# Kernel optimization log

Measured on AMD Instinct MI355X. Metric: run time of the kernel, lower is better.

The kernel has to match this reference:

```python
import jax, jax.numpy as jnp
import numpy as np

B, S, D, H = 2, 2048, 1024, 16
DH = D // H
SCALE = 1.0 / float(np.sqrt(DH))


def setup_inputs() -> dict:
    key = jax.random.key(0)
    ks = jax.random.split(key, 9)
    std = 1.0 / float(np.sqrt(D))
    x = jax.random.normal(ks[0], (B, S, D), dtype=jnp.float32)
    # causal mask: True = masked (future positions)
    mask = jnp.triu(jnp.ones((S, S), dtype=bool), k=1)
    Wq = jax.random.normal(ks[1], (D, D), dtype=jnp.float32) * std
    Wk = jax.random.normal(ks[2], (D, D), dtype=jnp.float32) * std
    Wv = jax.random.normal(ks[3], (D, D), dtype=jnp.float32) * std
    Wo = jax.random.normal(ks[4], (D, D), dtype=jnp.float32) * std
    bq = jax.random.normal(ks[5], (D,), dtype=jnp.float32) * 0.01
    bk = jax.random.normal(ks[6], (D,), dtype=jnp.float32) * 0.01
    bv = jax.random.normal(ks[7], (D,), dtype=jnp.float32) * 0.01
    bo = jax.random.normal(ks[8], (D,), dtype=jnp.float32) * 0.01
    return {"x": x, "mask": mask, "Wq": Wq, "bq": bq, "Wk": Wk, "bk": bk,
            "Wv": Wv, "bv": bv, "Wo": Wo, "bo": bo}


def _split_heads(t):
    # (B, S, D) -> (B, H, S, DH)
    return t.reshape(B, S, H, DH).transpose(0, 2, 1, 3)


def reference(x, mask, Wq, bq, Wk, bk, Wv, bv, Wo, bo):
    # torch nn.Linear: y = x @ W.T + b
    q = _split_heads(x @ Wq.T + bq)
    k = _split_heads(x @ Wk.T + bk)
    v = _split_heads(x @ Wv.T + bv)
    # scores: (B, H, S, S)
    scores = jnp.einsum('bhsd,bhtd->bhst', q, k) * SCALE
    scores = jnp.where(mask[None, None, :, :], jnp.float32(-1e9), scores)
    attn = jax.nn.softmax(scores, axis=-1)
    attn = jnp.nan_to_num(attn, nan=0.0)
    out = jnp.einsum('bhst,bhtd->bhsd', attn, v)
    out = out.transpose(0, 2, 1, 3).reshape(B, S, D)
    return out @ Wo.T + bo
```

## Files before the change

kernel.cpp:

```cpp
#include <hip/hip_runtime.h>

#define S_LEN  2048
#define DMODEL 1024
#define NHEAD  16
#define DHEAD  64
#define SCALE_F 0.125f

typedef unsigned short ushort_t;
typedef __attribute__((ext_vector_type(8))) short bf16x8;
typedef __attribute__((ext_vector_type(4))) float f32x4;

typedef __attribute__((address_space(1))) void gv_t;
typedef __attribute__((address_space(3))) void lv_t;

__device__ __forceinline__ ushort_t f2bf(float f) {
    unsigned u = __builtin_bit_cast(unsigned, f);
    unsigned r = (u + 0x7FFFu + ((u >> 16) & 1u)) >> 16;
    return (ushort_t)r;
}

__device__ __forceinline__ void gload16(const ushort_t* g, ushort_t* l) {
    __builtin_amdgcn_global_load_lds((gv_t*)g, (lv_t*)l, 16, 0, 0);
}

__global__ void cast_all(const float* __restrict__ x,
                         const float* __restrict__ Wq, const float* __restrict__ Wk,
                         const float* __restrict__ Wv, const float* __restrict__ Wo,
                         ushort_t* __restrict__ dst, int n4) {
    int i = blockIdx.x * blockDim.x + threadIdx.x;
    int stride = gridDim.x * blockDim.x;
    for (int idx = i; idx < n4; idx += stride) {
        const float* src; int off;
        if (idx < 1048576)      { src = x;  off = idx; }
        else if (idx < 1310720) { src = Wq; off = idx - 1048576; }
        else if (idx < 1572864) { src = Wk; off = idx - 1310720; }
        else if (idx < 1835008) { src = Wv; off = idx - 1572864; }
        else                    { src = Wo; off = idx - 1835008; }
        float4 f = ((const float4*)src)[off];
        ushort4 o;
        o.x = f2bf(f.x); o.y = f2bf(f.y); o.z = f2bf(f.z); o.w = f2bf(f.w);
        ((ushort4*)dst)[idx] = o;
    }
}

template<int MODE, int BM>
__launch_bounds__(256)
__global__ void gemm_bt(const ushort_t* __restrict__ A, const ushort_t* __restrict__ Bw,
                        const float* __restrict__ b0, const float* __restrict__ b1,
                        const float* __restrict__ b2,
                        void* __restrict__ out0, void* __restrict__ out1, void* __restrict__ out2,
                        int M, int N, int K) {
    constexpr int MF = BM / 32;
    __shared__ ushort_t As[2][BM][32];
    __shared__ ushort_t Bs[2][128][32];
    const int tid  = threadIdx.x;
    const int lane = tid & 63;
    const int w    = tid >> 6;
    const int wr   = w >> 1, wc = w & 1;
    const int m0   = blockIdx.x * BM;
    const int n0   = blockIdx.y * 128;
    const int l15  = lane & 15;
    const int lg   = lane >> 4;
    const int srow = lane >> 2;
    const int scol = (lane & 3) * 8;

    f32x4 acc[MF][4] = {};

    auto stage = [&](int buf, int k0) {
#pragma unroll
        for (int j = 0; j < BM / 64; j++) {
            const int rbase = w * (BM / 4) + j * 16;
            gload16(A + (size_t)(m0 + rbase + srow) * K + k0 + scol, &As[buf][rbase][0]);
        }
#pragma unroll
        for (int j = 0; j < 2; j++) {
            const int rbase = w * 32 + j * 16;
            gload16(Bw + (size_t)(n0 + rbase + srow) * K + k0 + scol, &Bs[buf][rbase][0]);
        }
    };

    stage(0, 0);
    __syncthreads();
    int buf = 0;

    for (int k0 = 0; k0 < K; k0 += 32) {
        if (k0 + 32 < K) stage(buf ^ 1, k0 + 32);
        bf16x8 af[MF], bfr[4];
#pragma unroll
        for (int i = 0; i < MF; i++) af[i]  = *(const bf16x8*)&As[buf][wr*(BM/2) + i*16 + l15][lg*8];
#pragma unroll
        for (int i = 0; i < 4;  i++) bfr[i] = *(const bf16x8*)&Bs[buf][wc*64 + i*16 + l15][lg*8];
#pragma unroll
        for (int mf = 0; mf < MF; mf++)
#pragma unroll
            for (int nf = 0; nf < 4; nf++)
                acc[mf][nf] = __builtin_amdgcn_mfma_f32_16x16x32_bf16(af[mf], bfr[nf], acc[mf][nf], 0, 0, 0);
        __syncthreads();
        buf ^= 1;
    }

#pragma unroll
    for (int mf = 0; mf < MF; mf++) {
#pragma unroll
        for (int nf = 0; nf < 4; nf++) {
            const int col = n0 + wc*64 + nf*16 + l15;
            if constexpr (MODE == 2) {
                const float bv = b0[col];
#pragma unroll
                for (int r = 0; r < 4; r++) {
                    const int row = m0 + wr*(BM/2) + mf*16 + lg*4 + r;
                    ((float*)out0)[(size_t)row * N + col] = acc[mf][nf][r] + bv;
                }
            } else {
                const int mat = col >> 10;
                const int c   = col & 1023;
                const int h   = c >> 6, dh = c & 63;
                const float* bp = (mat == 0) ? b0 : ((mat == 1) ? b1 : b2);
                const float bv = bp[c];
#pragma unroll
                for (int r = 0; r < 4; r++) {
                    const int row = m0 + wr*(BM/2) + mf*16 + lg*4 + r;
                    const int b = row >> 11, s = row & 2047;
                    const float v = acc[mf][nf][r] + bv;
                    if (mat == 0)
                        ((ushort_t*)out0)[((size_t)(b*NHEAD + h) * S_LEN + s) * DHEAD + dh] = f2bf(v);
                    else if (mat == 1)
                        ((ushort_t*)out1)[((size_t)(b*NHEAD + h) * S_LEN + s) * DHEAD + dh] = f2bf(v);
                    else
                        ((ushort_t*)out2)[((size_t)(b*NHEAD + h) * DHEAD + dh) * S_LEN + s] = f2bf(v);
                }
            }
        }
    }
}

__launch_bounds__(256, 3)
__global__ void attn_fwd(const ushort_t* __restrict__ Q, const ushort_t* __restrict__ Kh,
                         const ushort_t* __restrict__ Vt, ushort_t* __restrict__ Aout) {
    __shared__ ushort_t Ks[2][64][64];
    __shared__ ushort_t Vs[2][64][64];
    __shared__ ushort_t Ps[4][16][72];
    const int tid  = threadIdx.x;
    const int lane = tid & 63;
    const int w    = tid >> 6;
    const int l15  = lane & 15, lg = lane >> 4;
    const int bh   = blockIdx.y;
    const int qta  = blockIdx.x;
    const int qtb  = 31 - qta;
    const size_t qkbase = (size_t)bh * S_LEN * DHEAD;
    const size_t vtbase = (size_t)bh * DHEAD * S_LEN;
    const float SL2E = SCALE_F * 1.44269504f;

    const int rsub = lane >> 3;
    const int csw  = ((lane & 7) ^ rsub) * 8;
    const int swz  = (l15 & 7) * 8;

    const int qa = qta * 64 + w * 16;
    const int qb = qtb * 64 + w * 16;

    bf16x8 aqA[2], aqB[2];
#pragma unroll
    for (int kc = 0; kc < 2; kc++) {
        aqA[kc] = *(const bf16x8*)(Q + qkbase + (size_t)(qa + l15) * DHEAD + kc*32 + lg*8);
        aqB[kc] = *(const bf16x8*)(Q + qkbase + (size_t)(qb + l15) * DHEAD + kc*32 + lg*8);
    }

    float mA = -3.0e38f, lA = 0.0f, mB = -3.0e38f, lB = 0.0f;
    f32x4 oA[4] = {}, oB[4] = {};

    auto stage = [&](int buf, int t) {
        const int kv0 = t * 64;
        const ushort_t* kp = Kh + qkbase + (size_t)kv0 * DHEAD;
        const ushort_t* vp = Vt + vtbase + kv0;
#pragma unroll
        for (int j2 = 0; j2 < 2; j2++) {
            const int j  = w * 2 + j2;
            const int rg = j * 8 + rsub;
            gload16(kp + (size_t)rg * DHEAD + csw, &Ks[buf][j*8][0]);
            gload16(vp + (size_t)rg * S_LEN + csw, &Vs[buf][j*8][0]);
        }
    };

    auto compute = [&](int buf, int t, int qbase, bf16x8 (&aq)[2], float& m, float& l,
                       f32x4 (&o)[4], bool domask) {
        const int kv0  = t * 64;
        const int rowq = qbase + l15;
        f32x4 sacc[4] = {};
        __builtin_amdgcn_s_setprio(1);
#pragma unroll
        for (int kc = 0; kc < 2; kc++)
#pragma unroll
            for (int nf = 0; nf < 4; nf++) {
                bf16x8 bk = *(const bf16x8*)&Ks[buf][nf*16 + l15][(kc*32 + lg*8) ^ swz];
                sacc[nf] = __builtin_amdgcn_mfma_f32_16x16x32_bf16(bk, aq[kc], sacc[nf], 0, 0, 0);
            }
        __builtin_amdgcn_s_setprio(0);

        float mx = -3.0e38f;
        if (domask) {
#pragma unroll
            for (int nf = 0; nf < 4; nf++)
#pragma unroll
                for (int r = 0; r < 4; r++) {
                    const int colk = kv0 + nf*16 + lg*4 + r;
                    float v = sacc[nf][r] * SL2E;
                    v = (colk > rowq) ? -3.0e38f : v;
                    sacc[nf][r] = v;
                    mx = fmaxf(mx, v);
                }
        } else {
#pragma unroll
            for (int nf = 0; nf < 4; nf++)
#pragma unroll
                for (int r = 0; r < 4; r++) {
                    const float v = sacc[nf][r] * SL2E;
                    sacc[nf][r] = v;
                    mx = fmaxf(mx, v);
                }
        }
        mx = fmaxf(mx, __shfl_xor(mx, 16));
        mx = fmaxf(mx, __shfl_xor(mx, 32));

        const bool skip = __all(mx <= m + 8.0f);
        const float mn = skip ? m : fmaxf(m, mx);

        float s = 0.0f;
#pragma unroll
        for (int nf = 0; nf < 4; nf++) {
            ushort_t pk[4];
#pragma unroll
            for (int r = 0; r < 4; r++) {
                const float p = exp2f(sacc[nf][r] - mn);
                s += p;
                pk[r] = f2bf(p);
            }
            *(ushort4*)&Ps[w][l15][nf*16 + lg*4] = *(ushort4*)pk;
        }
        s += __shfl_xor(s, 16);
        s += __shfl_xor(s, 32);

        if (skip) {
            l += s;
        } else {
            const float corr = exp2f(m - mn);
            m = mn;
            l = l * corr + s;
            float cf[4];
#pragma unroll
            for (int r = 0; r < 4; r++) cf[r] = __shfl(corr, lg*4 + r);
#pragma unroll
            for (int nf = 0; nf < 4; nf++)
#pragma unroll
                for (int r = 0; r < 4; r++) o[nf][r] *= cf[r];
        }

        __builtin_amdgcn_s_setprio(1);
#pragma unroll
        for (int kc = 0; kc < 2; kc++) {
            bf16x8 pa = *(const bf16x8*)&Ps[w][l15][kc*32 + lg*8];
#pragma unroll
            for (int nf = 0; nf < 4; nf++) {
                bf16x8 bv = *(const bf16x8*)&Vs[buf][nf*16 + l15][(kc*32 + lg*8) ^ swz];
                o[nf] = __builtin_amdgcn_mfma_f32_16x16x32_bf16(pa, bv, o[nf], 0, 0, 0);
            }
        }
        __builtin_amdgcn_s_setprio(0);
    };

    stage(0, 0);
    __syncthreads();
    int buf = 0;

    for (int t = 0; t <= qta; t++) {
        if (t < qtb) stage(buf ^ 1, t + 1);
        compute(buf, t, qa, aqA, mA, lA, oA, t == qta);
        compute(buf, t, qb, aqB, mB, lB, oB, false);
        __syncthreads();
        buf ^= 1;
    }
    for (int t = qta + 1; t <= qtb; t++) {
        if (t < qtb) stage(buf ^ 1, t + 1);
        compute(buf, t, qb, aqB, mB, lB, oB, t == qtb);
        __syncthreads();
        buf ^= 1;
    }

    const int b = bh >> 4, h = bh & 15;
    const float invA = 1.0f / lA, invB = 1.0f / lB;
#pragma unroll
    for (int r = 0; r < 4; r++) {
        const float ia = __shfl(invA, lg*4 + r);
        const float ib = __shfl(invB, lg*4 + r);
        const int rowa = qa + lg*4 + r;
        const int rowb = qb + lg*4 + r;
#pragma unroll
        for (int nf = 0; nf < 4; nf++) {
            Aout[((size_t)(b * S_LEN) + rowa) * DMODEL + h*DHEAD + nf*16 + l15] = f2bf(oA[nf][r] * ia);
            Aout[((size_t)(b * S_LEN) + rowb) * DMODEL + h*DHEAD + nf*16 + l15] = f2bf(oB[nf][r] * ib);
        }
    }
}

extern "C" void kernel_launch(void* const* d_in, const int* in_sizes, int n_in,
                              void* d_out, int out_size, void* d_ws, size_t ws_size,
                              hipStream_t stream) {
    (void)in_sizes; (void)n_in; (void)out_size; (void)ws_size;
    const float* x  = (const float*)d_in[0];
    const float* Wq = (const float*)d_in[2];
    const float* bq = (const float*)d_in[3];
    const float* Wk = (const float*)d_in[4];
    const float* bk = (const float*)d_in[5];
    const float* Wv = (const float*)d_in[6];
    const float* bv = (const float*)d_in[7];
    const float* Wo = (const float*)d_in[8];
    const float* bo = (const float*)d_in[9];

    char* ws = (char*)d_ws;
    ushort_t* xb    = (ushort_t*)(ws);
    ushort_t* Wqkvb = (ushort_t*)(ws + (8u  << 20));
    ushort_t* Wob   = (ushort_t*)(ws + (14u << 20));
    ushort_t* Qh    = (ushort_t*)(ws + (16u << 20));
    ushort_t* Kh    = (ushort_t*)(ws + (24u << 20));
    ushort_t* Vth   = (ushort_t*)(ws + (32u << 20));
    ushort_t* Ao    = (ushort_t*)(ws + (40u << 20));

    cast_all<<<2048, 256, 0, stream>>>(x, Wq, Wk, Wv, Wo, xb, 2097152);

    gemm_bt<0, 128><<<dim3(32, 24), 256, 0, stream>>>(xb, Wqkvb, bq, bk, bv,
                                                      Qh, Kh, Vth, 2*S_LEN, 3*DMODEL, DMODEL);

    attn_fwd<<<dim3(16, 2*NHEAD), 256, 0, stream>>>(Qh, Kh, Vth, Ao);

    gemm_bt<2, 64><<<dim3(64, 8), 256, 0, stream>>>(Ao, Wob, bo, nullptr, nullptr,
                                                    d_out, nullptr, nullptr, 2*S_LEN, DMODEL, DMODEL);
}
```

Before: 127.7 us.

## Split paired causal query tiles into separate blocks with interleaved scheduling

The attention kernel previously gave each block two query tiles (a and 31-a) to balance causal work. It now launches one block per query tile on a 32x32 grid, ordering tiles so heavy and light ones alternate, and raises the occupancy hint to 4. The softmax scale times log2(e) is folded into Q inside the QKV GEMM epilogue. The P tile drops its padding in favour of an XOR swizzle, and P is packed with v_cvt_pk_bf16_f32. Each block now reloads K/V for its own tile instead of sharing them across two tiles, and the order in which blocks are dispatched now decides load balance.

```diff
diff --git a/kernel.cpp b/kernel.cpp
--- a/kernel.cpp
+++ b/kernel.cpp
@@ -5,6 +5,7 @@
 #define NHEAD  16
 #define DHEAD  64
 #define SCALE_F 0.125f
+#define SL2E_F 0.180336880f
 
 typedef unsigned short ushort_t;
 typedef __attribute__((ext_vector_type(8))) short bf16x8;
@@ -17,6 +18,12 @@
     unsigned u = __builtin_bit_cast(unsigned, f);
     unsigned r = (u + 0x7FFFu + ((u >> 16) & 1u)) >> 16;
     return (ushort_t)r;
+}
+
+__device__ __forceinline__ unsigned cvtpk_bf16(float a, float b) {
+    unsigned r;
+    asm("v_cvt_pk_bf16_f32 %0, %1, %2" : "=v"(r) : "v"(a), "v"(b));
+    return r;
 }
 
 __device__ __forceinline__ void gload16(const ushort_t* g, ushort_t* l) {
@@ -121,10 +128,11 @@
                 for (int r = 0; r < 4; r++) {
                     const int row = m0 + wr*(BM/2) + mf*16 + lg*4 + r;
                     const int b = row >> 11, s = row & 2047;
-                    const float v = acc[mf][nf][r] + bv;
-                    if (mat == 0)
+                    float v = acc[mf][nf][r] + bv;
+                    if (mat == 0) {
+                        v *= SL2E_F;
                         ((ushort_t*)out0)[((size_t)(b*NHEAD + h) * S_LEN + s) * DHEAD + dh] = f2bf(v);
-                    else if (mat == 1)
+                    } else if (mat == 1)
                         ((ushort_t*)out1)[((size_t)(b*NHEAD + h) * S_LEN + s) * DHEAD + dh] = f2bf(v);
                     else
                         ((ushort_t*)out2)[((size_t)(b*NHEAD + h) * DHEAD + dh) * S_LEN + s] = f2bf(v);
@@ -134,39 +142,39 @@
     }
 }
 
-__launch_bounds__(256, 3)
+__launch_bounds__(256, 4)
 __global__ void attn_fwd(const ushort_t* __restrict__ Q, const ushort_t* __restrict__ Kh,
                          const ushort_t* __restrict__ Vt, ushort_t* __restrict__ Aout) {
     __shared__ ushort_t Ks[2][64][64];
     __shared__ ushort_t Vs[2][64][64];
-    __shared__ ushort_t Ps[4][16][72];
+    __shared__ ushort_t Ps[4][16][64];
     const int tid  = threadIdx.x;
     const int lane = tid & 63;
     const int w    = tid >> 6;
     const int l15  = lane & 15, lg = lane >> 4;
-    const int bh   = blockIdx.y;
-    const int qta  = blockIdx.x;
-    const int qtb  = 31 - qta;
+    const int bh   = blockIdx.x;
+    const int y    = blockIdx.y;
+    const int kq   = y >> 3, g0 = y & 7;
+    const int qt   = (kq == 0) ? 2*g0 : (kq == 1) ? (31 - 2*g0)
+                   : (kq == 2) ? (2*g0 + 1) : (30 - 2*g0);
+
     const size_t qkbase = (size_t)bh * S_LEN * DHEAD;
     const size_t vtbase = (size_t)bh * DHEAD * S_LEN;
-    const float SL2E = SCALE_F * 1.44269504f;
-
-    const int rsub = lane >> 3;
-    const int csw  = ((lane & 7) ^ rsub) * 8;
-    const int swz  = (l15 & 7) * 8;
-
-    const int qa = qta * 64 + w * 16;
-    const int qb = qtb * 64 + w * 16;
-
-    bf16x8 aqA[2], aqB[2];
-#pragma unroll
-    for (int kc = 0; kc < 2; kc++) {
-        aqA[kc] = *(const bf16x8*)(Q + qkbase + (size_t)(qa + l15) * DHEAD + kc*32 + lg*8);
-        aqB[kc] = *(const bf16x8*)(Q + qkbase + (size_t)(qb + l15) * DHEAD + kc*32 + lg*8);
-    }
-
-    float mA = -3.0e38f, lA = 0.0f, mB = -3.0e38f, lB = 0.0f;
-    f32x4 oA[4] = {}, oB[4] = {};
+
+    const int rsub  = lane >> 3;
+    const int csw   = ((lane & 7) ^ rsub) * 8;
+    const int swz   = (l15 & 7) * 8;
+    const int psxor = (l15 & 7) << 4;
+
+    const int qw = qt * 64 + w * 16;
+
+    bf16x8 aq[2];
+#pragma unroll
+    for (int kc = 0; kc < 2; kc++)
+        aq[kc] = *(const bf16x8*)(Q + qkbase + (size_t)(qw + l15) * DHEAD + kc*32 + lg*8);
+
+    float m = -3.0e38f, l = 0.0f;
+    f32x4 o[4] = {};
 
     auto stage = [&](int buf, int t) {
         const int kv0 = t * 64;
@@ -181,10 +189,16 @@
         }
     };
 
-    auto compute = [&](int buf, int t, int qbase, bf16x8 (&aq)[2], float& m, float& l,
-                       f32x4 (&o)[4], bool domask) {
-        const int kv0  = t * 64;
-        const int rowq = qbase + l15;
+    ushort_t* psw = &Ps[w][0][0];
+    char* psrow = (char*)(psw + l15 * 64);
+
+    stage(0, 0);
+    __syncthreads();
+    int buf = 0;
+
+    for (int t = 0; t <= qt; t++) {
+        if (t < qt) stage(buf ^ 1, t + 1);
+
         f32x4 sacc[4] = {};
         __builtin_amdgcn_s_setprio(1);
 #pragma unroll
@@ -196,46 +210,43 @@
             }
         __builtin_amdgcn_s_setprio(0);
 
-        float mx = -3.0e38f;
-        if (domask) {
+        if (t == qt) {
+            const int rowq = qw + l15;
+            const int kv0  = t * 64;
 #pragma unroll
             for (int nf = 0; nf < 4; nf++)
 #pragma unroll
                 for (int r = 0; r < 4; r++) {
                     const int colk = kv0 + nf*16 + lg*4 + r;
-                    float v = sacc[nf][r] * SL2E;
-                    v = (colk > rowq) ? -3.0e38f : v;
-                    sacc[nf][r] = v;
-                    mx = fmaxf(mx, v);
+                    if (colk > rowq) sacc[nf][r] = -3.0e38f;
                 }
-        } else {
-#pragma unroll
-            for (int nf = 0; nf < 4; nf++)
-#pragma unroll
-                for (int r = 0; r < 4; r++) {
-                    const float v = sacc[nf][r] * SL2E;
-                    sacc[nf][r] = v;
-                    mx = fmaxf(mx, v);
-                }
-        }
+        }
+
+        float mnf[4];
+#pragma unroll
+        for (int nf = 0; nf < 4; nf++)
+            mnf[nf] = fmaxf(fmaxf(sacc[nf][0], sacc[nf][1]), fmaxf(sacc[nf][2], sacc[nf][3]));
+        float mx = fmaxf(fmaxf(mnf[0], mnf[1]), fmaxf(mnf[2], mnf[3]));
         mx = fmaxf(mx, __shfl_xor(mx, 16));
         mx = fmaxf(mx, __shfl_xor(mx, 32));
 
         const bool skip = __all(mx <= m + 8.0f);
         const float mn = skip ? m : fmaxf(m, mx);
 
-        float s = 0.0f;
+        float snf[4];
 #pragma unroll
         for (int nf = 0; nf < 4; nf++) {
-            ushort_t pk[4];
-#pragma unroll
-            for (int r = 0; r < 4; r++) {
-                const float p = exp2f(sacc[nf][r] - mn);
-                s += p;
-                pk[r] = f2bf(p);
-            }
-            *(ushort4*)&Ps[w][l15][nf*16 + lg*4] = *(ushort4*)pk;
-        }
+            const float p0 = exp2f(sacc[nf][0] - mn);
+            const float p1 = exp2f(sacc[nf][1] - mn);
+            const float p2 = exp2f(sacc[nf][2] - mn);
+            const float p3 = exp2f(sacc[nf][3] - mn);
+            uint2 pk;
+            pk.x = cvtpk_bf16(p0, p1);
+            pk.y = cvtpk_bf16(p2, p3);
+            *(uint2*)(psrow + (((nf*16 + lg*4) * 2) ^ psxor)) = pk;
+            snf[nf] = (p0 + p1) + (p2 + p3);
+        }
+        float s = (snf[0] + snf[1]) + (snf[2] + snf[3]);
         s += __shfl_xor(s, 16);
         s += __shfl_xor(s, 32);
 
@@ -257,7 +268,7 @@
         __builtin_amdgcn_s_setprio(1);
 #pragma unroll
         for (int kc = 0; kc < 2; kc++) {
-            bf16x8 pa = *(const bf16x8*)&Ps[w][l15][kc*32 + lg*8];
+            bf16x8 pa = *(const bf16x8*)(psrow + (((kc*32 + lg*8) * 2) ^ psxor));
 #pragma unroll
             for (int nf = 0; nf < 4; nf++) {
                 bf16x8 bv = *(const bf16x8*)&Vs[buf][nf*16 + l15][(kc*32 + lg*8) ^ swz];
@@ -265,39 +276,20 @@
             }
         }
         __builtin_amdgcn_s_setprio(0);
-    };
-
-    stage(0, 0);
-    __syncthreads();
-    int buf = 0;
-
-    for (int t = 0; t <= qta; t++) {
-        if (t < qtb) stage(buf ^ 1, t + 1);
-        compute(buf, t, qa, aqA, mA, lA, oA, t == qta);
-        compute(buf, t, qb, aqB, mB, lB, oB, false);
+
         __syncthreads();
         buf ^= 1;
     }
-    for (int t = qta + 1; t <= qtb; t++) {
-        if (t < qtb) stage(buf ^ 1, t + 1);
-        compute(buf, t, qb, aqB, mB, lB, oB, t == qtb);
-        __syncthreads();
-        buf ^= 1;
-    }
 
     const int b = bh >> 4, h = bh & 15;
-    const float invA = 1.0f / lA, invB = 1.0f / lB;
+    const float inv = 1.0f / l;
 #pragma unroll
     for (int r = 0; r < 4; r++) {
-        const float ia = __shfl(invA, lg*4 + r);
-        const float ib = __shfl(invB, lg*4 + r);
-        const int rowa = qa + lg*4 + r;
-        const int rowb = qb + lg*4 + r;
-#pragma unroll
-        for (int nf = 0; nf < 4; nf++) {
-            Aout[((size_t)(b * S_LEN) + rowa) * DMODEL + h*DHEAD + nf*16 + l15] = f2bf(oA[nf][r] * ia);
-            Aout[((size_t)(b * S_LEN) + rowb) * DMODEL + h*DHEAD + nf*16 + l15] = f2bf(oB[nf][r] * ib);
-        }
+        const float ia = __shfl(inv, lg*4 + r);
+        const int rowq = qw + lg*4 + r;
+#pragma unroll
+        for (int nf = 0; nf < 4; nf++)
+            Aout[((size_t)(b * S_LEN) + rowq) * DMODEL + h*DHEAD + nf*16 + l15] = f2bf(o[nf][r] * ia);
     }
 }
 
@@ -329,7 +321,7 @@
     gemm_bt<0, 128><<<dim3(32, 24), 256, 0, stream>>>(xb, Wqkvb, bq, bk, bv,
                                                       Qh, Kh, Vth, 2*S_LEN, 3*DMODEL, DMODEL);
 
-    attn_fwd<<<dim3(16, 2*NHEAD), 256, 0, stream>>>(Qh, Kh, Vth, Ao);
+    attn_fwd<<<dim3(2*NHEAD, 32), 256, 0, stream>>>(Qh, Kh, Vth, Ao);
 
     gemm_bt<2, 64><<<dim3(64, 8), 256, 0, stream>>>(Ao, Wob, bo, nullptr, nullptr,
                                                     d_out, nullptr, nullptr, 2*S_LEN, DMODEL, DMODEL);
```

New measurement: 115.2 us. -9.8%, faster.
